# Performance work log

Hardware: AMD Instinct MI355X
Metric: run time of the kernel (lower is better)

## Reference

```python
import math
import jax, jax.numpy as jnp
import numpy as np

H = 1024
N2 = 32  # N // 2
L_LEN = 4096


def setup_inputs() -> dict:
    key = jax.random.key(0)
    k0, k1, k2 = jax.random.split(key, 3)
    log_dt = jax.random.uniform(k0, (H,), dtype=jnp.float32) * (
        math.log(0.1) - math.log(0.001)) + math.log(0.001)
    C_real = jax.random.normal(k1, (H, N2), dtype=jnp.float32)
    C_imag = jax.random.normal(k2, (H, N2), dtype=jnp.float32)
    log_A_real = jnp.log(0.5 * jnp.ones((H, N2), dtype=jnp.float32))
    A_imag = math.pi * jnp.tile(jnp.arange(N2, dtype=jnp.float32)[None, :], (H, 1))
    return {
        "log_dt": log_dt,
        "C_real": C_real,
        "C_imag": C_imag,
        "log_A_real": log_A_real,
        "A_imag": A_imag,
        "L": L_LEN,
    }


def reference(log_dt, C_real, C_imag, log_A_real, A_imag, L):
    dt = jnp.exp(log_dt)                                   # [H]
    A = -jnp.exp(log_A_real) + 1j * A_imag                 # [H, N2] complex
    dtA = A * dt[:, None]                                  # [H, N2]
    l = jnp.arange(L, dtype=jnp.float32)                   # [L]
    Kexp = jnp.exp(dtA[:, :, None] * l)                    # [H, N2, L] complex (Vandermonde)
    Ct = (C_real + 1j * C_imag) * (jnp.exp(dtA) - 1.0) / A  # [H, N2]
    K = 2.0 * jnp.einsum('hn,hnl->hl', Ct, Kexp).real      # [H, L]
    return K
```

## Files before the change

kernel.cpp:

```cpp
#include <hip/hip_runtime.h>


#define N2    32
#define NPAIR (N2 / 2)
#define LLEN  4096
#define BLK   256
#define CL    (LLEN / BLK)
#define PCH   4
#define TOL   1e-3f

typedef float v2f __attribute__((ext_vector_type(2)));

__global__ __launch_bounds__(BLK, 4) void s4d_kernel(
    const float* __restrict__ log_dt,
    const float* __restrict__ C_real,
    const float* __restrict__ C_imag,
    const float* __restrict__ log_A_real,
    const float* __restrict__ A_imag,
    float* __restrict__ out)
{
    const int h = blockIdx.x;
    const int t = threadIdx.x;

    __shared__ float4 sP[N2];
    __shared__ float4 sQ[N2];
    __shared__ v2f    s2A[NPAIR];
    __shared__ v2f    sMR2[NPAIR];
    __shared__ float  sUdr, sSA, sRmax;
    __shared__ int    sJcut, sFlag;

    if (t < N2) {
        const int n = t;
        const float dt = __expf(log_dt[h]);
        const float aR = -__expf(log_A_real[h * N2 + n]);
        const float aI = A_imag[h * N2 + n];
        const float dR = aR * dt;

        const double trev = (double)aI * (double)dt * 0.15915494309189535;
        const float  th   = (float)trev;
        const float  tl   = (float)(trev - (double)th);

        double pz = trev; pz -= floor(pz);
        const float e1 = __expf(dR);
        const float zr = e1 * __builtin_amdgcn_cosf((float)pz);
        const float zi = e1 * __builtin_amdgcn_sinf((float)pz);

        const float inv = 1.0f / (aR * aR + aI * aI);
        const float nr  = zr - 1.0f;
        const float qr  = (nr * aR + zi * aI) * inv;
        const float qi  = (zi * aR - nr * aI) * inv;
        const float c_r = C_real[h * N2 + n], c_i = C_imag[h * N2 + n];
        const float Ctr = c_r * qr - c_i * qi;
        const float Cti = c_r * qi + c_i * qr;

        double p256 = trev * 256.0; p256 -= floor(p256);
        const float ew = __expf(dR * 256.0f);
        const float wx = ew * __builtin_amdgcn_cosf((float)p256);
        const float wy = ew * __builtin_amdgcn_sinf((float)p256);
        const float r2 = ew * ew;
        const float drl2 = dR * 1.4426950408889634f;

        sP[n] = make_float4(th, tl, drl2, 1.0f / r2);
        sQ[n] = make_float4(Ctr, Cti, wx, wy);
        ((float*)s2A)[n]  = 2.0f * wx;
        ((float*)sMR2)[n] = -r2;

        float S = fabsf(Ctr) + fabsf(Cti);
        float r = ew;
#pragma unroll
        for (int m = 16; m >= 1; m >>= 1) {
            S += __shfl_xor(S, m, 32);
            r  = fmaxf(r, __shfl_xor(r, m, 32));
        }
        const float u = __shfl(drl2, 0, 32);
        const unsigned long long bal = __ballot(drl2 == u);
        if (n == 0) {
            sFlag = ((bal & 0xFFFFFFFFull) == 0xFFFFFFFFull) ? 1 : 0;
            sUdr  = u;
            sSA   = S;
            sRmax = r;
            int jc = CL;
            if (r < 0.9999f) {
                const float tail0 = 2.0f * S / (1.0f - r);
                jc = 0;
                float rj = 1.0f;
                while (jc < CL && tail0 * rj >= TOL) { rj *= r; ++jc; }
            }
            sJcut = jc;
        }
    }
    __syncthreads();

    v2f acc[CL];
#pragma unroll
    for (int j = 0; j < CL; ++j) acc[j] = (v2f){0.0f, 0.0f};

    const float tf    = (float)t;
    const int   jcut  = __builtin_amdgcn_readfirstlane(sJcut);
    const int   flagU = __builtin_amdgcn_readfirstlane(sFlag);

    bool  active = (jcut > 0);
    float erU    = 1.0f;
    if (flagU) {
        erU = __builtin_amdgcn_exp2f(sUdr * tf);
        if (sRmax < 0.9999f && 2.0f * sSA * erU / (1.0f - sRmax) < TOL)
            active = false;
    }

    if (active) {
        for (int p0 = 0; p0 < NPAIR; p0 += PCH) {
            v2f x[PCH], xm[PCH], c2a[PCH], cmr[PCH];

#pragma unroll
            for (int k = 0; k < PCH; ++k) {
                const int pair = p0 + k;
                c2a[k] = s2A[pair];
                cmr[k] = sMR2[pair];
#pragma unroll
                for (int e = 0; e < 2; ++e) {
                    const int n = 2 * pair + e;
                    const float4 P = sP[n];
                    const float4 Q = sQ[n];
                    const float er = flagU ? erU
                                           : __builtin_amdgcn_exp2f(P.z * tf);
                    const float p    = P.x * tf;
                    const float perr = __builtin_fmaf(P.x, tf, -p);
                    const float f    = __builtin_amdgcn_fractf(p)
                                     + __builtin_fmaf(P.y, tf, perr);
                    const float c = __builtin_amdgcn_cosf(f);
                    const float s = __builtin_amdgcn_sinf(f);
                    const float x0  = er * __builtin_fmaf(-Q.y, s, Q.x * c);
                    const float y0  = er * __builtin_fmaf( Q.y, c, Q.x * s);
                    const float xm1 = __builtin_fmaf(y0, Q.w, x0 * Q.z) * P.w;
                    if (e == 0) { x[k].x = x0; xm[k].x = xm1; }
                    else        { x[k].y = x0; xm[k].y = xm1; }
                }
            }

#pragma unroll
            for (int jp = 0; jp < CL / 2; ++jp) {
                if (2 * jp < jcut) {
#pragma unroll
                    for (int k = 0; k < PCH; ++k) {
                        acc[2 * jp] += x[k];
                        xm[k] = c2a[k] * x[k] + cmr[k] * xm[k];
                    }
#pragma unroll
                    for (int k = 0; k < PCH; ++k) {
                        acc[2 * jp + 1] += xm[k];
                        x[k] = c2a[k] * xm[k] + cmr[k] * x[k];
                    }
                }
            }
        }
    }

    float* __restrict__ o = out + (size_t)h * LLEN + t;
#pragma unroll
    for (int j = 0; j < CL; ++j) o[j * BLK] = 2.0f * (acc[j].x + acc[j].y);
}

extern "C" void kernel_launch(void* const* d_in, const int* in_sizes, int n_in,
                              void* d_out, int out_size, void* d_ws, size_t ws_size,
                              hipStream_t stream) {
    const float* log_dt     = (const float*)d_in[0];
    const float* C_real     = (const float*)d_in[1];
    const float* C_imag     = (const float*)d_in[2];
    const float* log_A_real = (const float*)d_in[3];
    const float* A_imag     = (const float*)d_in[4];
    float* out = (float*)d_out;

    const int H = in_sizes[0];
    s4d_kernel<<<dim3(H), dim3(BLK), 0, stream>>>(
        log_dt, C_real, C_imag, log_A_real, A_imag, out);
}
```

Before: 81.48 us.

## Factor per-thread Vandermonde seeds into shared 16x16 twiddle tables

Instead of each thread evaluating exp2, sin and cos for every mode to seed the recurrence, the block precomputes small shared tables: z^k for k<16, and Ct*z^(16m) and Ct*z^(16m+256) for m<16. Each thread then forms its two starting values with a complex multiply of table entries, t = t0 + 16*t1. The recurrence is restarted from x[0] and x[1] directly, without back-stepping, and the uniform-decay special case is replaced by a single bound using the maximum decay. This removes transcendental work from the hot loop at the cost of an extra table-build phase, a second barrier, and larger shared memory use.

```diff
diff --git a/kernel.cpp b/kernel.cpp
--- a/kernel.cpp
+++ b/kernel.cpp
@@ -22,12 +22,15 @@
     const int h = blockIdx.x;
     const int t = threadIdx.x;
 
-    __shared__ float4 sP[N2];
-    __shared__ float4 sQ[N2];
+    __shared__ v2f    sT0[N2][16];
+    __shared__ float4 sU1[N2][16];
     __shared__ v2f    s2A[NPAIR];
     __shared__ v2f    sMR2[NPAIR];
-    __shared__ float  sUdr, sSA, sRmax;
-    __shared__ int    sJcut, sFlag;
+    __shared__ v2f    sCt[N2];
+    __shared__ float  sDrl2[N2];
+    __shared__ double sTrev[N2];
+    __shared__ float  sS, sRmax, sDrmax;
+    __shared__ int    sJcut;
 
     if (t < N2) {
         const int n = t;
@@ -37,8 +40,6 @@
         const float dR = aR * dt;
 
         const double trev = (double)aI * (double)dt * 0.15915494309189535;
-        const float  th   = (float)trev;
-        const float  tl   = (float)(trev - (double)th);
 
         double pz = trev; pz -= floor(pz);
         const float e1 = __expf(dR);
@@ -56,29 +57,26 @@
         double p256 = trev * 256.0; p256 -= floor(p256);
         const float ew = __expf(dR * 256.0f);
         const float wx = ew * __builtin_amdgcn_cosf((float)p256);
-        const float wy = ew * __builtin_amdgcn_sinf((float)p256);
         const float r2 = ew * ew;
         const float drl2 = dR * 1.4426950408889634f;
 
-        sP[n] = make_float4(th, tl, drl2, 1.0f / r2);
-        sQ[n] = make_float4(Ctr, Cti, wx, wy);
+        sCt[n]   = (v2f){Ctr, Cti};
+        sDrl2[n] = drl2;
+        sTrev[n] = trev;
         ((float*)s2A)[n]  = 2.0f * wx;
         ((float*)sMR2)[n] = -r2;
 
         float S = fabsf(Ctr) + fabsf(Cti);
         float r = ew;
+        float dm = drl2;
 #pragma unroll
         for (int m = 16; m >= 1; m >>= 1) {
-            S += __shfl_xor(S, m, 32);
-            r  = fmaxf(r, __shfl_xor(r, m, 32));
-        }
-        const float u = __shfl(drl2, 0, 32);
-        const unsigned long long bal = __ballot(drl2 == u);
+            S  += __shfl_xor(S, m, 32);
+            r   = fmaxf(r,  __shfl_xor(r,  m, 32));
+            dm  = fmaxf(dm, __shfl_xor(dm, m, 32));
+        }
         if (n == 0) {
-            sFlag = ((bal & 0xFFFFFFFFull) == 0xFFFFFFFFull) ? 1 : 0;
-            sUdr  = u;
-            sSA   = S;
-            sRmax = r;
+            sS = S; sRmax = r; sDrmax = dm;
             int jc = CL;
             if (r < 0.9999f) {
                 const float tail0 = 2.0f * S / (1.0f - r);
@@ -91,25 +89,60 @@
     }
     __syncthreads();
 
+#pragma unroll
+    for (int it = 0; it < 4; ++it) {
+        const int tau = t + BLK * it;
+        if (tau < 512) {
+            const int n = tau >> 4, k = tau & 15;
+            double p = sTrev[n] * (double)k; p -= floor(p);
+            const float g = __builtin_amdgcn_exp2f(sDrl2[n] * (float)k);
+            sT0[n][k] = (v2f){ g * __builtin_amdgcn_cosf((float)p),
+                               g * __builtin_amdgcn_sinf((float)p) };
+        } else {
+            const int tu = tau - 512;
+            const int n = tu >> 4, m = tu & 15;
+            const v2f    Ct = sCt[n];
+            const double tr = sTrev[n];
+            const float  dl = sDrl2[n];
+
+            double p0 = tr * (double)(16 * m); p0 -= floor(p0);
+            const float g0 = __builtin_amdgcn_exp2f(dl * (float)(16 * m));
+            const float c0 = g0 * __builtin_amdgcn_cosf((float)p0);
+            const float s0 = g0 * __builtin_amdgcn_sinf((float)p0);
+
+            double p1 = tr * (double)(16 * m + 256); p1 -= floor(p1);
+            const float g1 = __builtin_amdgcn_exp2f(dl * (float)(16 * m + 256));
+            const float c1 = g1 * __builtin_amdgcn_cosf((float)p1);
+            const float s1 = g1 * __builtin_amdgcn_sinf((float)p1);
+
+            sU1[n][m] = make_float4(Ct.x * c0 - Ct.y * s0,
+                                    Ct.x * s0 + Ct.y * c0,
+                                    Ct.x * c1 - Ct.y * s1,
+                                    Ct.x * s1 + Ct.y * c1);
+        }
+    }
+    __syncthreads();
+
     v2f acc[CL];
 #pragma unroll
     for (int j = 0; j < CL; ++j) acc[j] = (v2f){0.0f, 0.0f};
 
-    const float tf    = (float)t;
-    const int   jcut  = __builtin_amdgcn_readfirstlane(sJcut);
-    const int   flagU = __builtin_amdgcn_readfirstlane(sFlag);
-
-    bool  active = (jcut > 0);
-    float erU    = 1.0f;
-    if (flagU) {
-        erU = __builtin_amdgcn_exp2f(sUdr * tf);
-        if (sRmax < 0.9999f && 2.0f * sSA * erU / (1.0f - sRmax) < TOL)
-            active = false;
+    const int jcut = __builtin_amdgcn_readfirstlane(sJcut);
+    bool active = (jcut > 0);
+    {
+        const float rmax = sRmax;
+        if (rmax < 0.9999f) {
+            const float bound = 2.0f * sS *
+                __builtin_amdgcn_exp2f(sDrmax * (float)t) / (1.0f - rmax);
+            if (bound < TOL) active = false;
+        }
     }
 
     if (active) {
+        const int t0 = t & 15, t1 = t >> 4;
+
         for (int p0 = 0; p0 < NPAIR; p0 += PCH) {
-            v2f x[PCH], xm[PCH], c2a[PCH], cmr[PCH];
+            v2f xa[PCH], xb[PCH], c2a[PCH], cmr[PCH];
 
 #pragma unroll
             for (int k = 0; k < PCH; ++k) {
@@ -119,36 +152,35 @@
 #pragma unroll
                 for (int e = 0; e < 2; ++e) {
                     const int n = 2 * pair + e;
-                    const float4 P = sP[n];
-                    const float4 Q = sQ[n];
-                    const float er = flagU ? erU
-                                           : __builtin_amdgcn_exp2f(P.z * tf);
-                    const float p    = P.x * tf;
-                    const float perr = __builtin_fmaf(P.x, tf, -p);
-                    const float f    = __builtin_amdgcn_fractf(p)
-                                     + __builtin_fmaf(P.y, tf, perr);
-                    const float c = __builtin_amdgcn_cosf(f);
-                    const float s = __builtin_amdgcn_sinf(f);
-                    const float x0  = er * __builtin_fmaf(-Q.y, s, Q.x * c);
-                    const float y0  = er * __builtin_fmaf( Q.y, c, Q.x * s);
-                    const float xm1 = __builtin_fmaf(y0, Q.w, x0 * Q.z) * P.w;
-                    if (e == 0) { x[k].x = x0; xm[k].x = xm1; }
-                    else        { x[k].y = x0; xm[k].y = xm1; }
+                    const v2f    b = sT0[n][t0];
+                    const float4 u = sU1[n][t1];
+                    const float x0 = __builtin_fmaf(-u.y, b.y, u.x * b.x);
+                    const float x1 = __builtin_fmaf(-u.w, b.y, u.z * b.x);
+                    if (e == 0) { xa[k].x = x0; xb[k].x = x1; }
+                    else        { xa[k].y = x0; xb[k].y = x1; }
                 }
             }
 
 #pragma unroll
-            for (int jp = 0; jp < CL / 2; ++jp) {
-                if (2 * jp < jcut) {
+            for (int k = 0; k < PCH; ++k) acc[0] += xa[k];
+            if (jcut > 1) {
+#pragma unroll
+                for (int k = 0; k < PCH; ++k) acc[1] += xb[k];
+            }
+
+#pragma unroll
+            for (int jp = 0; jp < (CL - 2) / 2; ++jp) {
+                const int j = 2 + 2 * jp;
+                if (j < jcut) {
 #pragma unroll
                     for (int k = 0; k < PCH; ++k) {
-                        acc[2 * jp] += x[k];
-                        xm[k] = c2a[k] * x[k] + cmr[k] * xm[k];
+                        xa[k] = c2a[k] * xb[k] + cmr[k] * xa[k];
+                        acc[j] += xa[k];
                     }
 #pragma unroll
                     for (int k = 0; k < PCH; ++k) {
-                        acc[2 * jp + 1] += xm[k];
-                        x[k] = c2a[k] * xm[k] + cmr[k] * x[k];
+                        xb[k] = c2a[k] * xa[k] + cmr[k] * xb[k];
+                        acc[j + 1] += xb[k];
                     }
                 }
             }
```

Measured after the change: 78.14 us. 1.04x faster.
